# Kernel tuning notes

Measured on AMD Instinct MI355X. Metric: run time of the kernel, lower is better.

Reference implementation:

```python
import jax, jax.numpy as jnp
import numpy as np

TOP_K = 30
NUM_RBF = 16
MAX_REL = 32  # max_relative_feature
EDGE_FEATURES = 128
NUM_PE = 16
EDGE_IN = NUM_PE + NUM_RBF * 25  # 416

B, L = 8, 1024


def setup_inputs() -> dict:
    key = jax.random.key(0)
    ks = jax.random.split(key, 8)
    X = jax.random.normal(ks[0], (B, L, 4, 3), dtype=jnp.float32)
    mask = jnp.ones((B, L), dtype=jnp.float32)
    residue_idx = jnp.arange(B * L, dtype=jnp.int64 if jax.config.jax_enable_x64 else jnp.int32).reshape(B, L) % L
    chain_labels = jnp.sort(jax.random.randint(ks[1], (B, L), 0, 4), axis=-1)
    # learned params
    W_pe = jax.random.normal(ks[2], (NUM_PE, 2 * MAX_REL + 2), dtype=jnp.float32) * 0.05
    b_pe = jnp.zeros((NUM_PE,), dtype=jnp.float32)
    W_edge = jax.random.normal(ks[3], (EDGE_FEATURES, EDGE_IN), dtype=jnp.float32) * 0.05
    ln_w = jnp.ones((EDGE_FEATURES,), dtype=jnp.float32)
    ln_b = jnp.zeros((EDGE_FEATURES,), dtype=jnp.float32)
    return {"X": X, "mask": mask, "residue_idx": residue_idx, "chain_labels": chain_labels,
            "W_pe": W_pe, "b_pe": b_pe, "W_edge": W_edge, "ln_w": ln_w, "ln_b": ln_b}


def reference(X, mask, residue_idx, chain_labels, W_pe, b_pe, W_edge, ln_w, ln_b):
    Bn, Ln = mask.shape
    # virtual C-beta from ideal geometry
    b = X[:, :, 1] - X[:, :, 0]
    c = X[:, :, 2] - X[:, :, 1]
    a = jnp.cross(b, c)
    Cb = -0.58273431 * a + 0.56802827 * b - 0.54067466 * c + X[:, :, 1]
    X5 = jnp.concatenate([X, Cb[:, :, None, :]], axis=2)  # [B,L,5,3]

    # kNN on CA-CA distances
    Ca = X5[:, :, 1]  # [B,L,3]
    m2 = mask[:, None, :] * mask[:, :, None]
    dX = Ca[:, None, :, :] - Ca[:, :, None, :]
    D = m2 * jnp.sqrt(jnp.sum(dX * dX, -1) + 1e-6)  # [B,L,L]
    D_max = jnp.max(D, -1, keepdims=True)
    D_adjust = D + (1.0 - m2) * D_max
    k = min(TOP_K, Ln)
    neg_vals, E_idx = jax.lax.top_k(-D_adjust, k)  # smallest-k

    # gather neighbor coords once: [B,L,K,5,3]
    batch = jnp.arange(Bn)[:, None, None]
    Xn = X5[batch, E_idx]
    # all 25 atom-pair distances to neighbors, fused: [B,L,K,5,5]
    diff = X5[:, :, None, :, None, :] - Xn[:, :, :, None, :, :]
    D_ab = jnp.sqrt(jnp.sum(diff * diff, -1) + 1e-6)
    # RBF featurization
    mu = jnp.linspace(2.0, 22.0, NUM_RBF)
    sigma = (22.0 - 2.0) / NUM_RBF
    RBF = jnp.exp(-(((D_ab[..., None] - mu) / sigma) ** 2))  # [B,L,K,5,5,16]
    # loop order in torch is c1-major, c2-minor, rbf innermost -> plain reshape matches
    RBF_all = RBF.reshape(Bn, Ln, k, 5 * 5 * NUM_RBF)

    # positional encodings
    offset = residue_idx[:, :, None] - residue_idx[:, None, :]
    offset_n = jnp.take_along_axis(offset, E_idx, axis=2)  # [B,L,K]
    d_chains = (chain_labels[:, :, None] == chain_labels[:, None, :]).astype(jnp.int32)
    E_chains = jnp.take_along_axis(d_chains, E_idx, axis=2)
    d = jnp.clip(offset_n + MAX_REL, 0, 2 * MAX_REL) * E_chains + (1 - E_chains) * (2 * MAX_REL + 1)
    d_onehot = jax.nn.one_hot(d, 2 * MAX_REL + 2, dtype=W_pe.dtype)
    E_pos = d_onehot @ W_pe.T + b_pe  # [B,L,K,16]

    E = jnp.concatenate([E_pos, RBF_all], axis=-1)  # [B,L,K,416]
    E = E @ W_edge.T  # edge_embedding, no bias
    # LayerNorm (eps=1e-5)
    mu_e = jnp.mean(E, -1, keepdims=True)
    var_e = jnp.var(E, -1, keepdims=True)
    E = (E - mu_e) / jnp.sqrt(var_e + 1e-5) * ln_w + ln_b
    return E, E_idx, X
```

## Files before the change

### kernel.cpp

```cpp
#include <hip/hip_runtime.h>
#include <math.h>

#define B_   8
#define L_   1024
#define K_   30
#define EF_  128
#define EIN_ 416
#define MAXREL_ 32

using f32x4 = __attribute__((ext_vector_type(4))) float;



__device__ __forceinline__ unsigned long long shflx64(unsigned long long v, int m)
{
    int lo = __shfl_xor((int)(unsigned)(v & 0xffffffffull), m, 64);
    int hi = __shfl_xor((int)(unsigned)(v >> 32), m, 64);
    return ((unsigned long long)(unsigned)hi << 32) | (unsigned)lo;
}

__global__ __launch_bounds__(256) void pf_pre_topk(
    const float* __restrict__ X, const float* __restrict__ W_pe,
    const float* __restrict__ b_pe, const float* __restrict__ W_edge,
    float* __restrict__ x5p, float* __restrict__ tpe, short* __restrict__ wt8s,
    float* __restrict__ outX, float* __restrict__ outEidxF)
{
    __shared__ float ca[L_ * 3];
    __shared__ unsigned long long hds[4][64];
    __shared__ unsigned long long sv[4][128];
    __shared__ unsigned long long tsh[4];
    __shared__ int cnt_s[4];

    int t = threadIdx.x;

    if (blockIdx.x >= 2048) {
        int id = (blockIdx.x - 2048) * 256 + t;

        if (id < B_ * L_ * 12) outX[id] = X[id];

        int id1 = id - B_ * L_ * 12;
        if (id1 >= 0 && id1 < B_ * L_) {
            const float* xp = X + (size_t)id1 * 12;
            float n0 = xp[0], n1 = xp[1], n2 = xp[2];
            float ca0 = xp[3], ca1 = xp[4], ca2 = xp[5];
            float c0 = xp[6], c1 = xp[7], c2 = xp[8];
            float o0 = xp[9], o1 = xp[10], o2 = xp[11];
            float bv0 = ca0 - n0, bv1 = ca1 - n1, bv2 = ca2 - n2;
            float cv0 = c0 - ca0, cv1 = c1 - ca1, cv2 = c2 - ca2;
            float av0 = bv1 * cv2 - bv2 * cv1;
            float av1 = bv2 * cv0 - bv0 * cv2;
            float av2 = bv0 * cv1 - bv1 * cv0;
            float cb0 = -0.58273431f * av0 + 0.56802827f * bv0 - 0.54067466f * cv0 + ca0;
            float cb1 = -0.58273431f * av1 + 0.56802827f * bv1 - 0.54067466f * cv1 + ca1;
            float cb2 = -0.58273431f * av2 + 0.56802827f * bv2 - 0.54067466f * cv2 + ca2;
            float* o = x5p + (size_t)id1 * 16;
            o[0] = n0;  o[1] = n1;  o[2] = n2;
            o[3] = ca0; o[4] = ca1; o[5] = ca2;
            o[6] = c0;  o[7] = c1;  o[8] = c2;
            o[9] = o0;  o[10] = o1; o[11] = o2;
            o[12] = cb0; o[13] = cb1; o[14] = cb2; o[15] = 0.f;
        }

        int id2 = id1 - B_ * L_;
        if (id2 >= 0 && id2 < 66 * 128) {
            int dcol = id2 >> 7, f = id2 & 127;
            const float* wrow = W_edge + (size_t)f * EIN_;
            float s = 0.f;
            #pragma unroll
            for (int p = 0; p < 16; p++) s += wrow[p] * W_pe[p * 66 + dcol];
            float sb = 0.f;
            #pragma unroll
            for (int p = 0; p < 16; p++) sb += wrow[p] * b_pe[p];
            tpe[id2] = (s + sb) * 8.0f;
        }

        int id3 = id2 - 66 * 128;
        if (id3 >= 0 && id3 < 128 * 208) {
            int f = id3 / 208, kp = (id3 - f * 208) * 2;
            float w0 = W_edge[(size_t)f * EIN_ + 16 + kp] * 8.0f;
            float w1 = W_edge[(size_t)f * EIN_ + 16 + kp + 1] * 8.0f;
            int pk = __builtin_amdgcn_cvt_pk_fp8_f32(w0, w1, 0, false);
            wt8s[f * 208 + (kp >> 1)] = (short)pk;
        }
        return;
    }

    int blk = blockIdx.x;
    int b = blk >> 8;
    const float* xb = X + (size_t)b * L_ * 12;

    for (int j = t; j < L_; j += 256) {
        ca[j * 3 + 0] = xb[j * 12 + 3];
        ca[j * 3 + 1] = xb[j * 12 + 4];
        ca[j * 3 + 2] = xb[j * 12 + 5];
    }
    __syncthreads();

    int w = t >> 6, lane = t & 63;
    int row = blk * 4 + w;
    int i = row & 1023;
    float cx = ca[i * 3 + 0], cy = ca[i * 3 + 1], cz = ca[i * 3 + 2];

    unsigned long long keys[16];
    #pragma unroll
    for (int kq = 0; kq < 16; kq++) {
        int j = lane + 64 * kq;
        float dx = ca[j * 3 + 0] - cx;
        float dy = ca[j * 3 + 1] - cy;
        float dz = ca[j * 3 + 2] - cz;
        float s = __fadd_rn(__fadd_rn(__fadd_rn(__fmul_rn(dx, dx), __fmul_rn(dy, dy)),
                                      __fmul_rn(dz, dz)), 1e-6f);
        float d = sqrtf(s);
        unsigned db = __builtin_bit_cast(unsigned, d);
        keys[kq] = ((unsigned long long)db << 10) | (unsigned)j;
    }

    unsigned long long tr[8];
    #pragma unroll
    for (int kq = 0; kq < 8; kq++)
        tr[kq] = keys[kq] < keys[kq + 8] ? keys[kq] : keys[kq + 8];
    #pragma unroll
    for (int st = 4; st >= 1; st >>= 1)
        #pragma unroll
        for (int kq = 0; kq < st; kq++)
            tr[kq] = tr[kq] < tr[kq + st] ? tr[kq] : tr[kq + st];

    unsigned long long mine = tr[0];
    hds[w][lane] = mine;
    if (lane == 0) cnt_s[w] = 0;
    __asm__ volatile("s_waitcnt lgkmcnt(0)" ::: "memory");
    int rk = 0;
    #pragma unroll 8
    for (int m = 0; m < 64; m++) rk += (hds[w][m] < mine) ? 1 : 0;
    if (rk == 29) tsh[w] = mine;
    __asm__ volatile("s_waitcnt lgkmcnt(0)" ::: "memory");
    unsigned long long T = tsh[w];

    int cnt = 0;
    #pragma unroll
    for (int kq = 0; kq < 16; kq++) cnt += (keys[kq] <= T) ? 1 : 0;
    int o = atomicAdd(&cnt_s[w], cnt);
    #pragma unroll
    for (int kq = 0; kq < 16; kq++) {
        if (keys[kq] <= T && o < 128) { sv[w][o] = keys[kq]; o++; }
    }
    __asm__ volatile("s_waitcnt lgkmcnt(0)" ::: "memory");
    int C = cnt_s[w];

    if (C <= 128) {
        unsigned long long a  = (lane < C)      ? sv[w][lane]      : ~0ull;
        unsigned long long b2 = (lane + 64 < C) ? sv[w][lane + 64] : ~0ull;
        int ra = 0, rb = 0;
        for (int m = 0; m < C; m++) {
            unsigned long long s = sv[w][m];
            ra += (s < a) ? 1 : 0;
            rb += (s < b2) ? 1 : 0;
        }
        if (lane < C && ra < K_)
            outEidxF[(size_t)row * K_ + ra] = (float)(unsigned)(a & 1023ull);
        if (lane + 64 < C && rb < K_)
            outEidxF[(size_t)row * K_ + rb] = (float)(unsigned)(b2 & 1023ull);
    } else {
        #pragma unroll 1
        for (int it = 0; it < K_; it++) {
            unsigned long long m = keys[0];
            #pragma unroll
            for (int kq = 1; kq < 16; kq++) m = keys[kq] < m ? keys[kq] : m;
            #pragma unroll
            for (int off = 1; off < 64; off <<= 1) {
                unsigned long long o2 = shflx64(m, off);
                m = o2 < m ? o2 : m;
            }
            if (lane == 0)
                outEidxF[(size_t)row * K_ + it] = (float)(unsigned)(m & 1023ull);
            #pragma unroll
            for (int kq = 0; kq < 16; kq++)
                keys[kq] = (keys[kq] == m) ? ~0ull : keys[kq];
        }
    }
}

__global__ __launch_bounds__(256, 5) void pf_edge(
    const float* __restrict__ x5p, const float* __restrict__ tpe,
    const unsigned char* __restrict__ wt8, const float* __restrict__ eidxF,
    const int* __restrict__ ridx, const int* __restrict__ chain,
    const float* __restrict__ ln_w, const float* __restrict__ ln_b,
    float* __restrict__ outE)
{
    __shared__ __align__(16) unsigned char featA8[64 * 424];
    __shared__ __align__(16) float xbuf[960];
    __shared__ __align__(16) float x5c[32];
    __shared__ int dpe_s[64];

    int t = threadIdx.x;
    int lane = t & 63, w = t >> 6;
    int q = lane >> 4, m15 = lane & 15;
    int row0 = blockIdx.x * 2;
    int b = row0 >> 10;

    if (t < 60) {
        int r = t >= 30, e = t - r * 30;
        int rowg = row0 + r;
        int j = (int)eidxF[(size_t)rowg * K_ + e];
        int off = ridx[rowg] - ridx[b * L_ + j];
        int same = (chain[rowg] == chain[b * L_ + j]);
        int dv = off + MAXREL_;
        dv = dv < 0 ? 0 : (dv > 2 * MAXREL_ ? 2 * MAXREL_ : dv);
        dpe_s[t + (r ? 2 : 0)] = same ? dv : (2 * MAXREL_ + 1);
    }
    if (t >= 60 && t < 64) {
        int p = t - 60;
        dpe_s[p < 2 ? 30 + p : 60 + p] = 0;
    }
    if (t < 240) {
        int e = t >> 2, c = t & 3;
        int r = e >= 30, ee = e - r * 30;
        int rowg = row0 + r;
        int j = (int)eidxF[(size_t)rowg * K_ + ee];
        ((float4*)xbuf)[e * 4 + c] = ((const float4*)x5p)[(size_t)(b * L_ + j) * 4 + c];
    } else if (t < 248) {
        int c = t - 240;
        ((float4*)x5c)[c] = ((const float4*)x5p)[(size_t)(row0 + (c >> 2)) * 4 + (c & 3)];
    }
    {
        int m = t >> 2, c = t & 3;
        *(int*)&featA8[m * 424 + 400 + c * 4] = 0;
    }
    __syncthreads();

    f32x4 acc[2][2];
    #pragma unroll
    for (int et = 0; et < 2; et++) {
        int m = et * 16 + m15;
        const float4* trow = (const float4*)(tpe + dpe_s[m] * 128);
        #pragma unroll
        for (int ft = 0; ft < 2; ft++) {
            float4 v = trow[w * 8 + ft * 4 + q];
            acc[et][ft][0] = v.x; acc[et][ft][1] = v.y;
            acc[et][ft][2] = v.z; acc[et][ft][3] = v.w;
        }
    }
    f32x4 acc2[2][2];
    #pragma unroll
    for (int et = 0; et < 2; et++) {
        int m = (et + 2) * 16 + m15;
        const float4* trow = (const float4*)(tpe + dpe_s[m] * 128);
        #pragma unroll
        for (int ft = 0; ft < 2; ft++) {
            float4 v = trow[w * 8 + ft * 4 + q];
            acc2[et][ft][0] = v.x; acc2[et][ft][1] = v.y;
            acc2[et][ft][2] = v.z; acc2[et][ft][3] = v.w;
        }
    }

    if (t < 250) {
        int p = t % 25, e0 = t / 25;
        int A = p / 5, Bv = p - A * 5;
        const int pb = p * 16;
        #pragma unroll
        for (int i = 0; i < 6; i++) {
            int e = e0 + 10 * i;
            int rr = (e >= 30);
            const float* xc = x5c + rr * 16 + A * 3;
            const float* xn = xbuf + e * 16 + Bv * 3;
            float dx = xc[0] - xn[0];
            float dy = xc[1] - xn[1];
            float dz = xc[2] - xn[2];
            float d = sqrtf(dx * dx + dy * dy + dz * dz + 1e-6f);
            d = fminf(d, 25.0f);
            float t8v = 0.8f * d - 10.1333333f;
            float t7v = t8v + 1.0666667f;
            float base8 = __expf(-t8v * t8v);
            float u     = __expf(2.1333333f * t8v);
            float base7 = __expf(-t7v * t7v);
            float uinv  = __builtin_amdgcn_rcpf(u);
            float wdn   = uinv * 0.10273980f;
            float vv[16];
            vv[8] = base8;
            float pp = base8;
            pp *= u;   vv[9]  = pp * 0.32053053f;
            pp *= u;   vv[10] = pp * 0.010555467f;
            pp *= u;   vv[11] = pp * 3.571282e-5f;
            pp *= u;   vv[12] = pp * 1.2413945e-8f;
            pp *= u;   vv[13] = pp * 4.4333619e-13f;
            pp *= u;   vv[14] = pp * 1.6266628e-18f;
            pp *= u;   vv[15] = pp * 6.1319565e-25f;
            vv[7] = base7;
            float qq = base7;
            qq *= wdn; vv[6]  = qq * 0.32053053f;
            qq *= wdn; vv[5]  = qq * 0.010555467f;
            qq *= wdn; vv[4]  = qq * 3.571282e-5f;
            qq *= wdn; vv[3]  = qq * 1.2413945e-8f;
            qq *= wdn; vv[2]  = qq * 4.4333619e-13f;
            qq *= wdn; vv[1]  = qq * 1.6266628e-18f;
            qq *= wdn; vv[0]  = qq * 6.1319565e-25f;
            int slot = e + (rr ? 2 : 0);
            int p0 = __builtin_amdgcn_cvt_pk_fp8_f32(vv[0], vv[1], 0, false);
            p0     = __builtin_amdgcn_cvt_pk_fp8_f32(vv[2], vv[3], p0, true);
            int p1 = __builtin_amdgcn_cvt_pk_fp8_f32(vv[4], vv[5], 0, false);
            p1     = __builtin_amdgcn_cvt_pk_fp8_f32(vv[6], vv[7], p1, true);
            int p2 = __builtin_amdgcn_cvt_pk_fp8_f32(vv[8], vv[9], 0, false);
            p2     = __builtin_amdgcn_cvt_pk_fp8_f32(vv[10], vv[11], p2, true);
            int p3 = __builtin_amdgcn_cvt_pk_fp8_f32(vv[12], vv[13], 0, false);
            p3     = __builtin_amdgcn_cvt_pk_fp8_f32(vv[14], vv[15], p3, true);
            long lo = (unsigned)p0 | ((long)(unsigned)p1 << 32);
            long hi = (unsigned)p2 | ((long)(unsigned)p3 << 32);
            *(long*)&featA8[slot * 424 + pb] = lo;
            *(long*)&featA8[slot * 424 + pb + 8] = hi;
        }
    }
    __syncthreads();

    for (int k0 = 0; k0 < 416; k0 += 32) {
        long ffr[4];
        #pragma unroll
        for (int et = 0; et < 4; et++)
            ffr[et] = *(const long*)&featA8[(et * 16 + m15) * 424 + k0 + q * 8];
        long wfr[2];
        #pragma unroll
        for (int ft = 0; ft < 2; ft++)
            wfr[ft] = *(const long*)&wt8[(size_t)(w * 32 + ft * 16 + m15) * 416 + k0 + q * 8];
        #pragma unroll
        for (int et = 0; et < 2; et++)
            #pragma unroll
            for (int ft = 0; ft < 2; ft++) {
                acc[et][ft] = __builtin_amdgcn_mfma_f32_16x16x32_fp8_fp8(
                    wfr[ft], ffr[et], acc[et][ft], 0, 0, 0);
                acc2[et][ft] = __builtin_amdgcn_mfma_f32_16x16x32_fp8_fp8(
                    wfr[ft], ffr[et + 2], acc2[et][ft], 0, 0, 0);
            }
    }

    float2* part = (float2*)xbuf;
    #pragma unroll
    for (int et = 0; et < 4; et++) {
        const f32x4* a0 = (et < 2) ? &acc[et][0] : &acc2[et - 2][0];
        float sv = 0.f, qv = 0.f;
        #pragma unroll
        for (int ft = 0; ft < 2; ft++)
            #pragma unroll
            for (int r = 0; r < 4; r++) {
                float v = a0[ft][r];
                sv += v; qv += v * v;
            }
        sv += __shfl_xor(sv, 16u, 64);
        qv += __shfl_xor(qv, 16u, 64);
        sv += __shfl_xor(sv, 32u, 64);
        qv += __shfl_xor(qv, 32u, 64);
        if (q == 0) part[(et * 16 + m15) * 4 + w] = make_float2(sv, qv);
    }
    __syncthreads();

    float2* muinv = (float2*)(xbuf + 512);
    if (t < 64) {
        float s = 0.f, s2 = 0.f;
        #pragma unroll
        for (int c = 0; c < 4; c++) {
            float2 pc = part[t * 4 + c];
            s += pc.x; s2 += pc.y;
        }
        float mu = s * (1.0f / 128.0f);
        float var = s2 * (1.0f / 128.0f) - mu * mu;
        var = var < 0.f ? 0.f : var;
        muinv[t] = make_float2(mu, rsqrtf(var + 6.4e-4f));
    }
    __syncthreads();

    float4 lwv[2], lbv[2];
    #pragma unroll
    for (int ft = 0; ft < 2; ft++) {
        lwv[ft] = ((const float4*)ln_w)[w * 8 + ft * 4 + q];
        lbv[ft] = ((const float4*)ln_b)[w * 8 + ft * 4 + q];
    }
    #pragma unroll
    for (int et = 0; et < 4; et++) {
        const f32x4* a0 = (et < 2) ? &acc[et][0] : &acc2[et - 2][0];
        int m = et * 16 + m15;
        if ((m & 31) < 30) {
            float2 mi = muinv[m];
            int rowg = row0 + (m >> 5);
            int eidx = m & 31;
            float* dst = outE + ((size_t)rowg * K_ + eidx) * 128 + w * 32 + q * 4;
            #pragma unroll
            for (int ft = 0; ft < 2; ft++) {
                float ax = mi.y * lwv[ft].x, ay = mi.y * lwv[ft].y;
                float az = mi.y * lwv[ft].z, aw = mi.y * lwv[ft].w;
                float4 o;
                o.x = a0[ft][0] * ax + (lbv[ft].x - mi.x * ax);
                o.y = a0[ft][1] * ay + (lbv[ft].y - mi.x * ay);
                o.z = a0[ft][2] * az + (lbv[ft].z - mi.x * az);
                o.w = a0[ft][3] * aw + (lbv[ft].w - mi.x * aw);
                *(float4*)(dst + ft * 16) = o;
            }
        }
    }
}

extern "C" void kernel_launch(void* const* d_in, const int* in_sizes, int n_in,
                              void* d_out, int out_size, void* d_ws, size_t ws_size,
                              hipStream_t stream)
{
    const float* X      = (const float*)d_in[0];
    const int*   ridx   = (const int*)d_in[2];
    const int*   chain  = (const int*)d_in[3];
    const float* W_pe   = (const float*)d_in[4];
    const float* b_pe   = (const float*)d_in[5];
    const float* W_edge = (const float*)d_in[6];
    const float* ln_w   = (const float*)d_in[7];
    const float* ln_b   = (const float*)d_in[8];

    float* outE    = (float*)d_out;
    float* outEidx = outE + (size_t)B_ * L_ * K_ * EF_;
    float* outX    = outEidx + (size_t)B_ * L_ * K_;

    float* x5p  = (float*)d_ws;
    float* tpe  = x5p + B_ * L_ * 16;
    short* wt8s = (short*)(tpe + 66 * 128);

    pf_pre_topk<<<2601, 256, 0, stream>>>(X, W_pe, b_pe, W_edge, x5p, tpe, wt8s,
                                          outX, outEidx);
    pf_edge<<<B_ * L_ / 2, 256, 0, stream>>>(x5p, tpe, (const unsigned char*)wt8s,
                                             outEidx, ridx, chain, ln_w, ln_b, outE);
}
```

Baseline: 197.4 us.

## Fuse kNN top-k selection into edge kernel and compute neighbor coords on the fly

Moves the per-row top-k neighbour search into the edge-feature kernel, so each block selects neighbours for its two rows and keeps the indices in shared memory instead of reading them back from global memory. The virtual C-beta coordinates are computed directly from X for each gathered neighbour, which removes the x5p workspace buffer. A small prep kernel still builds the positional table and the FP8 weights. In exchange, every block reloads all 1024 CA coordinates of its batch and only two of its four waves do the top-k work. Shared memory is reused across the two phases, and the occupancy hint drops from 5 to 4 blocks.

```diff
diff --git a/kernel.cpp b/kernel.cpp
--- a/kernel.cpp
+++ b/kernel.cpp
@@ -19,208 +19,207 @@
     return ((unsigned long long)(unsigned)hi << 32) | (unsigned)lo;
 }
 
-__global__ __launch_bounds__(256) void pf_pre_topk(
-    const float* __restrict__ X, const float* __restrict__ W_pe,
-    const float* __restrict__ b_pe, const float* __restrict__ W_edge,
-    float* __restrict__ x5p, float* __restrict__ tpe, short* __restrict__ wt8s,
-    float* __restrict__ outX, float* __restrict__ outEidxF)
+__device__ __forceinline__ void make_x5(const float* __restrict__ xp,
+                                        float* __restrict__ o)
 {
-    __shared__ float ca[L_ * 3];
-    __shared__ unsigned long long hds[4][64];
-    __shared__ unsigned long long sv[4][128];
-    __shared__ unsigned long long tsh[4];
-    __shared__ int cnt_s[4];
-
-    int t = threadIdx.x;
-
-    if (blockIdx.x >= 2048) {
-        int id = (blockIdx.x - 2048) * 256 + t;
-
-        if (id < B_ * L_ * 12) outX[id] = X[id];
-
-        int id1 = id - B_ * L_ * 12;
-        if (id1 >= 0 && id1 < B_ * L_) {
-            const float* xp = X + (size_t)id1 * 12;
-            float n0 = xp[0], n1 = xp[1], n2 = xp[2];
-            float ca0 = xp[3], ca1 = xp[4], ca2 = xp[5];
-            float c0 = xp[6], c1 = xp[7], c2 = xp[8];
-            float o0 = xp[9], o1 = xp[10], o2 = xp[11];
-            float bv0 = ca0 - n0, bv1 = ca1 - n1, bv2 = ca2 - n2;
-            float cv0 = c0 - ca0, cv1 = c1 - ca1, cv2 = c2 - ca2;
-            float av0 = bv1 * cv2 - bv2 * cv1;
-            float av1 = bv2 * cv0 - bv0 * cv2;
-            float av2 = bv0 * cv1 - bv1 * cv0;
-            float cb0 = -0.58273431f * av0 + 0.56802827f * bv0 - 0.54067466f * cv0 + ca0;
-            float cb1 = -0.58273431f * av1 + 0.56802827f * bv1 - 0.54067466f * cv1 + ca1;
-            float cb2 = -0.58273431f * av2 + 0.56802827f * bv2 - 0.54067466f * cv2 + ca2;
-            float* o = x5p + (size_t)id1 * 16;
-            o[0] = n0;  o[1] = n1;  o[2] = n2;
-            o[3] = ca0; o[4] = ca1; o[5] = ca2;
-            o[6] = c0;  o[7] = c1;  o[8] = c2;
-            o[9] = o0;  o[10] = o1; o[11] = o2;
-            o[12] = cb0; o[13] = cb1; o[14] = cb2; o[15] = 0.f;
-        }
-
-        int id2 = id1 - B_ * L_;
-        if (id2 >= 0 && id2 < 66 * 128) {
-            int dcol = id2 >> 7, f = id2 & 127;
-            const float* wrow = W_edge + (size_t)f * EIN_;
-            float s = 0.f;
-            #pragma unroll
-            for (int p = 0; p < 16; p++) s += wrow[p] * W_pe[p * 66 + dcol];
-            float sb = 0.f;
-            #pragma unroll
-            for (int p = 0; p < 16; p++) sb += wrow[p] * b_pe[p];
-            tpe[id2] = (s + sb) * 8.0f;
-        }
-
-        int id3 = id2 - 66 * 128;
-        if (id3 >= 0 && id3 < 128 * 208) {
-            int f = id3 / 208, kp = (id3 - f * 208) * 2;
-            float w0 = W_edge[(size_t)f * EIN_ + 16 + kp] * 8.0f;
-            float w1 = W_edge[(size_t)f * EIN_ + 16 + kp + 1] * 8.0f;
-            int pk = __builtin_amdgcn_cvt_pk_fp8_f32(w0, w1, 0, false);
-            wt8s[f * 208 + (kp >> 1)] = (short)pk;
-        }
+    float n0 = xp[0], n1 = xp[1], n2 = xp[2];
+    float ca0 = xp[3], ca1 = xp[4], ca2 = xp[5];
+    float c0 = xp[6], c1 = xp[7], c2 = xp[8];
+    float o0 = xp[9], o1 = xp[10], o2 = xp[11];
+    float bv0 = ca0 - n0, bv1 = ca1 - n1, bv2 = ca2 - n2;
+    float cv0 = c0 - ca0, cv1 = c1 - ca1, cv2 = c2 - ca2;
+    float av0 = bv1 * cv2 - bv2 * cv1;
+    float av1 = bv2 * cv0 - bv0 * cv2;
+    float av2 = bv0 * cv1 - bv1 * cv0;
+    o[0] = n0;  o[1] = n1;  o[2] = n2;
+    o[3] = ca0; o[4] = ca1; o[5] = ca2;
+    o[6] = c0;  o[7] = c1;  o[8] = c2;
+    o[9] = o0;  o[10] = o1; o[11] = o2;
+    o[12] = -0.58273431f * av0 + 0.56802827f * bv0 - 0.54067466f * cv0 + ca0;
+    o[13] = -0.58273431f * av1 + 0.56802827f * bv1 - 0.54067466f * cv1 + ca1;
+    o[14] = -0.58273431f * av2 + 0.56802827f * bv2 - 0.54067466f * cv2 + ca2;
+    o[15] = 0.f;
+}
+
+__global__ __launch_bounds__(256) void pf_pre(
+    const float* __restrict__ W_pe, const float* __restrict__ b_pe,
+    const float* __restrict__ W_edge,
+    float* __restrict__ tpe, short* __restrict__ wt8s)
+{
+    int id = blockIdx.x * 256 + threadIdx.x;
+
+    if (id < 66 * 128) {
+        int dcol = id >> 7, f = id & 127;
+        const float* wrow = W_edge + (size_t)f * EIN_;
+        float s = 0.f;
+        #pragma unroll
+        for (int p = 0; p < 16; p++) s += wrow[p] * W_pe[p * 66 + dcol];
+        float sb = 0.f;
+        #pragma unroll
+        for (int p = 0; p < 16; p++) sb += wrow[p] * b_pe[p];
+        tpe[id] = (s + sb) * 8.0f;
         return;
     }
-
-    int blk = blockIdx.x;
-    int b = blk >> 8;
-    const float* xb = X + (size_t)b * L_ * 12;
-
-    for (int j = t; j < L_; j += 256) {
-        ca[j * 3 + 0] = xb[j * 12 + 3];
-        ca[j * 3 + 1] = xb[j * 12 + 4];
-        ca[j * 3 + 2] = xb[j * 12 + 5];
-    }
-    __syncthreads();
-
-    int w = t >> 6, lane = t & 63;
-    int row = blk * 4 + w;
-    int i = row & 1023;
-    float cx = ca[i * 3 + 0], cy = ca[i * 3 + 1], cz = ca[i * 3 + 2];
-
-    unsigned long long keys[16];
-    #pragma unroll
-    for (int kq = 0; kq < 16; kq++) {
-        int j = lane + 64 * kq;
-        float dx = ca[j * 3 + 0] - cx;
-        float dy = ca[j * 3 + 1] - cy;
-        float dz = ca[j * 3 + 2] - cz;
-        float s = __fadd_rn(__fadd_rn(__fadd_rn(__fmul_rn(dx, dx), __fmul_rn(dy, dy)),
-                                      __fmul_rn(dz, dz)), 1e-6f);
-        float d = sqrtf(s);
-        unsigned db = __builtin_bit_cast(unsigned, d);
-        keys[kq] = ((unsigned long long)db << 10) | (unsigned)j;
-    }
-
-    unsigned long long tr[8];
-    #pragma unroll
-    for (int kq = 0; kq < 8; kq++)
-        tr[kq] = keys[kq] < keys[kq + 8] ? keys[kq] : keys[kq + 8];
-    #pragma unroll
-    for (int st = 4; st >= 1; st >>= 1)
-        #pragma unroll
-        for (int kq = 0; kq < st; kq++)
-            tr[kq] = tr[kq] < tr[kq + st] ? tr[kq] : tr[kq + st];
-
-    unsigned long long mine = tr[0];
-    hds[w][lane] = mine;
-    if (lane == 0) cnt_s[w] = 0;
-    __asm__ volatile("s_waitcnt lgkmcnt(0)" ::: "memory");
-    int rk = 0;
-    #pragma unroll 8
-    for (int m = 0; m < 64; m++) rk += (hds[w][m] < mine) ? 1 : 0;
-    if (rk == 29) tsh[w] = mine;
-    __asm__ volatile("s_waitcnt lgkmcnt(0)" ::: "memory");
-    unsigned long long T = tsh[w];
-
-    int cnt = 0;
-    #pragma unroll
-    for (int kq = 0; kq < 16; kq++) cnt += (keys[kq] <= T) ? 1 : 0;
-    int o = atomicAdd(&cnt_s[w], cnt);
-    #pragma unroll
-    for (int kq = 0; kq < 16; kq++) {
-        if (keys[kq] <= T && o < 128) { sv[w][o] = keys[kq]; o++; }
-    }
-    __asm__ volatile("s_waitcnt lgkmcnt(0)" ::: "memory");
-    int C = cnt_s[w];
-
-    if (C <= 128) {
-        unsigned long long a  = (lane < C)      ? sv[w][lane]      : ~0ull;
-        unsigned long long b2 = (lane + 64 < C) ? sv[w][lane + 64] : ~0ull;
-        int ra = 0, rb = 0;
-        for (int m = 0; m < C; m++) {
-            unsigned long long s = sv[w][m];
-            ra += (s < a) ? 1 : 0;
-            rb += (s < b2) ? 1 : 0;
-        }
-        if (lane < C && ra < K_)
-            outEidxF[(size_t)row * K_ + ra] = (float)(unsigned)(a & 1023ull);
-        if (lane + 64 < C && rb < K_)
-            outEidxF[(size_t)row * K_ + rb] = (float)(unsigned)(b2 & 1023ull);
-    } else {
-        #pragma unroll 1
-        for (int it = 0; it < K_; it++) {
-            unsigned long long m = keys[0];
-            #pragma unroll
-            for (int kq = 1; kq < 16; kq++) m = keys[kq] < m ? keys[kq] : m;
-            #pragma unroll
-            for (int off = 1; off < 64; off <<= 1) {
-                unsigned long long o2 = shflx64(m, off);
-                m = o2 < m ? o2 : m;
-            }
-            if (lane == 0)
-                outEidxF[(size_t)row * K_ + it] = (float)(unsigned)(m & 1023ull);
-            #pragma unroll
-            for (int kq = 0; kq < 16; kq++)
-                keys[kq] = (keys[kq] == m) ? ~0ull : keys[kq];
-        }
+    int id3 = id - 66 * 128;
+    if (id3 < 128 * 208) {
+        int f = id3 / 208, kp = (id3 - f * 208) * 2;
+        float w0 = W_edge[(size_t)f * EIN_ + 16 + kp] * 8.0f;
+        float w1 = W_edge[(size_t)f * EIN_ + 16 + kp + 1] * 8.0f;
+        int pk = __builtin_amdgcn_cvt_pk_fp8_f32(w0, w1, 0, false);
+        wt8s[f * 208 + (kp >> 1)] = (short)pk;
     }
 }
 
-__global__ __launch_bounds__(256, 5) void pf_edge(
-    const float* __restrict__ x5p, const float* __restrict__ tpe,
-    const unsigned char* __restrict__ wt8, const float* __restrict__ eidxF,
+__global__ __launch_bounds__(256, 4) void pf_fused(
+    const float* __restrict__ X, const float* __restrict__ tpe,
+    const unsigned char* __restrict__ wt8,
     const int* __restrict__ ridx, const int* __restrict__ chain,
     const float* __restrict__ ln_w, const float* __restrict__ ln_b,
-    float* __restrict__ outE)
+    float* __restrict__ outE, float* __restrict__ outEidxF,
+    float* __restrict__ outX)
 {
-    __shared__ __align__(16) unsigned char featA8[64 * 424];
-    __shared__ __align__(16) float xbuf[960];
-    __shared__ __align__(16) float x5c[32];
-    __shared__ int dpe_s[64];
+    __shared__ __align__(16) unsigned char smem[31360];
+    __shared__ int nidx[2][32];
 
     int t = threadIdx.x;
     int lane = t & 63, w = t >> 6;
     int q = lane >> 4, m15 = lane & 15;
-    int row0 = blockIdx.x * 2;
+    int blk = blockIdx.x;
+    int row0 = blk * 2;
     int b = row0 >> 10;
+
+    if (t < 6) ((float4*)outX)[blk * 6 + t] = ((const float4*)X)[blk * 6 + t];
+
+    {
+        float* ca = (float*)smem;
+        unsigned long long* hds = (unsigned long long*)(smem + 12288);
+        unsigned long long* svv = (unsigned long long*)(smem + 13312);
+        unsigned long long* tsh = (unsigned long long*)(smem + 15360);
+        int* cnt_s = (int*)(smem + 15376);
+
+        const float* xb = X + (size_t)b * L_ * 12;
+        for (int j = t; j < L_; j += 256) {
+            ca[j * 3 + 0] = xb[j * 12 + 3];
+            ca[j * 3 + 1] = xb[j * 12 + 4];
+            ca[j * 3 + 2] = xb[j * 12 + 5];
+        }
+        __syncthreads();
+
+        if (w < 2) {
+            int row = row0 + w;
+            int i = row & 1023;
+            float cx = ca[i * 3 + 0], cy = ca[i * 3 + 1], cz = ca[i * 3 + 2];
+
+            unsigned long long keys[16];
+            #pragma unroll
+            for (int kq = 0; kq < 16; kq++) {
+                int j = lane + 64 * kq;
+                float dx = ca[j * 3 + 0] - cx;
+                float dy = ca[j * 3 + 1] - cy;
+                float dz = ca[j * 3 + 2] - cz;
+                float s = __fadd_rn(__fadd_rn(__fadd_rn(__fmul_rn(dx, dx),
+                              __fmul_rn(dy, dy)), __fmul_rn(dz, dz)), 1e-6f);
+                float d = sqrtf(s);
+                unsigned db = __builtin_bit_cast(unsigned, d);
+                keys[kq] = ((unsigned long long)db << 10) | (unsigned)j;
+            }
+
+            unsigned long long tr[8];
+            #pragma unroll
+            for (int kq = 0; kq < 8; kq++)
+                tr[kq] = keys[kq] < keys[kq + 8] ? keys[kq] : keys[kq + 8];
+            #pragma unroll
+            for (int st = 4; st >= 1; st >>= 1)
+                #pragma unroll
+                for (int kq = 0; kq < st; kq++)
+                    tr[kq] = tr[kq] < tr[kq + st] ? tr[kq] : tr[kq + st];
+
+            unsigned long long mine = tr[0];
+            hds[w * 64 + lane] = mine;
+            if (lane == 0) cnt_s[w] = 0;
+            __asm__ volatile("s_waitcnt lgkmcnt(0)" ::: "memory");
+            int rk = 0;
+            #pragma unroll 8
+            for (int m = 0; m < 64; m++) rk += (hds[w * 64 + m] < mine) ? 1 : 0;
+            if (rk == 29) tsh[w] = mine;
+            __asm__ volatile("s_waitcnt lgkmcnt(0)" ::: "memory");
+            unsigned long long T = tsh[w];
+
+            int cnt = 0;
+            #pragma unroll
+            for (int kq = 0; kq < 16; kq++) cnt += (keys[kq] <= T) ? 1 : 0;
+            int o = atomicAdd(&cnt_s[w], cnt);
+            #pragma unroll
+            for (int kq = 0; kq < 16; kq++) {
+                if (keys[kq] <= T && o < 128) { svv[w * 128 + o] = keys[kq]; o++; }
+            }
+            __asm__ volatile("s_waitcnt lgkmcnt(0)" ::: "memory");
+            int C = cnt_s[w];
+
+            if (C <= 128) {
+                unsigned long long a  = (lane < C)      ? svv[w * 128 + lane]      : ~0ull;
+                unsigned long long b2 = (lane + 64 < C) ? svv[w * 128 + lane + 64] : ~0ull;
+                int ra = 0, rb = 0;
+                for (int m = 0; m < C; m++) {
+                    unsigned long long s = svv[w * 128 + m];
+                    ra += (s < a) ? 1 : 0;
+                    rb += (s < b2) ? 1 : 0;
+                }
+                if (lane < C && ra < K_) {
+                    int j = (int)(unsigned)(a & 1023ull);
+                    outEidxF[(size_t)row * K_ + ra] = (float)j;
+                    nidx[w][ra] = j;
+                }
+                if (lane + 64 < C && rb < K_) {
+                    int j = (int)(unsigned)(b2 & 1023ull);
+                    outEidxF[(size_t)row * K_ + rb] = (float)j;
+                    nidx[w][rb] = j;
+                }
+            } else {
+                #pragma unroll 1
+                for (int it = 0; it < K_; it++) {
+                    unsigned long long m = keys[0];
+                    #pragma unroll
+                    for (int kq = 1; kq < 16; kq++) m = keys[kq] < m ? keys[kq] : m;
+                    #pragma unroll
+                    for (int off = 1; off < 64; off <<= 1) {
+                        unsigned long long o2 = shflx64(m, off);
+                        m = o2 < m ? o2 : m;
+                    }
+                    if (lane == 0) {
+                        int j = (int)(unsigned)(m & 1023ull);
+                        outEidxF[(size_t)row * K_ + it] = (float)j;
+                        nidx[w][it] = j;
+                    }
+                    #pragma unroll
+                    for (int kq = 0; kq < 16; kq++)
+                        keys[kq] = (keys[kq] == m) ? ~0ull : keys[kq];
+                }
+            }
+        }
+    }
+    __syncthreads();
+
+    unsigned char* featA8 = smem;
+    float* xbuf  = (float*)(smem + 27136);
+    float* x5c   = (float*)(smem + 30976);
+    int*   dpe_s = (int*)(smem + 31104);
 
     if (t < 60) {
         int r = t >= 30, e = t - r * 30;
         int rowg = row0 + r;
-        int j = (int)eidxF[(size_t)rowg * K_ + e];
+        int j = nidx[r][e];
         int off = ridx[rowg] - ridx[b * L_ + j];
         int same = (chain[rowg] == chain[b * L_ + j]);
         int dv = off + MAXREL_;
         dv = dv < 0 ? 0 : (dv > 2 * MAXREL_ ? 2 * MAXREL_ : dv);
         dpe_s[t + (r ? 2 : 0)] = same ? dv : (2 * MAXREL_ + 1);
-    }
-    if (t >= 60 && t < 64) {
-        int p = t - 60;
+        make_x5(X + (size_t)(b * L_ + j) * 12, xbuf + t * 16);
+    } else if (t < 62) {
+        make_x5(X + (size_t)(row0 + (t - 60)) * 12, x5c + (t - 60) * 16);
+    } else if (t < 66) {
+        int p = t - 62;
         dpe_s[p < 2 ? 30 + p : 60 + p] = 0;
-    }
-    if (t < 240) {
-        int e = t >> 2, c = t & 3;
-        int r = e >= 30, ee = e - r * 30;
-        int rowg = row0 + r;
-        int j = (int)eidxF[(size_t)rowg * K_ + ee];
-        ((float4*)xbuf)[e * 4 + c] = ((const float4*)x5p)[(size_t)(b * L_ + j) * 4 + c];
-    } else if (t < 248) {
-        int c = t - 240;
-        ((float4*)x5c)[c] = ((const float4*)x5p)[(size_t)(row0 + (c >> 2)) * 4 + (c & 3)];
     }
     {
         int m = t >> 2, c = t & 3;
@@ -413,12 +412,11 @@
     float* outEidx = outE + (size_t)B_ * L_ * K_ * EF_;
     float* outX    = outEidx + (size_t)B_ * L_ * K_;
 
-    float* x5p  = (float*)d_ws;
-    float* tpe  = x5p + B_ * L_ * 16;
+    float* tpe  = (float*)d_ws;
     short* wt8s = (short*)(tpe + 66 * 128);
 
-    pf_pre_topk<<<2601, 256, 0, stream>>>(X, W_pe, b_pe, W_edge, x5p, tpe, wt8s,
-                                          outX, outEidx);
-    pf_edge<<<B_ * L_ / 2, 256, 0, stream>>>(x5p, tpe, (const unsigned char*)wt8s,
-                                             outEidx, ridx, chain, ln_w, ln_b, outE);
+    pf_pre<<<137, 256, 0, stream>>>(W_pe, b_pe, W_edge, tpe, wt8s);
+    pf_fused<<<B_ * L_ / 2, 256, 0, stream>>>(
+        X, tpe, (const unsigned char*)wt8s, ridx, chain, ln_w, ln_b,
+        outE, outEidx, outX);
 }
```

Result: no change. 198.5 us (+0.5%).
